# Optimization experiments

Measured on AMD Instinct MI355X. Metric: run time of the kernel, lower is better.

Reference implementation:

```python
import jax, jax.numpy as jnp
import numpy as np

B, C_IN, C_OUT, H, W = 8, 4, 64, 8, 2048


def setup_inputs() -> dict:
    key = jax.random.key(0)
    ks = jax.random.split(key, 7)
    # torch Conv2d default init: U(-s, s) with s = 1/sqrt(fan_in), fan_in = C_in*1*1
    s = 1.0 / np.sqrt(C_IN)
    u = lambda k, shape: jax.random.uniform(k, shape, jnp.float32, -s, s)
    return {
        "x": jax.random.normal(ks[0], (B, C_IN, H, W), jnp.float32),
        "Wq": u(ks[1], (C_OUT, C_IN)), "bq": u(ks[2], (C_OUT,)),
        "Wk": u(ks[3], (C_OUT, C_IN)), "bk": u(ks[4], (C_OUT,)),
        "Wv": u(ks[5], (C_OUT, C_IN)), "bv": u(ks[6], (C_OUT,)),
        "causal": 1,
    }


def reference(x, Wq, bq, Wk, bk, Wv, bv, causal):
    b, c_in, h, w = x.shape
    # 1x1 conv == per-pixel linear over channel axis
    def proj(Wm, bm):
        y = jnp.einsum('bchw,oc->bohw', x, Wm) + bm[None, :, None, None]
        return y.reshape(b, -1, w)              # [B, C_out*H, W]
    Q = proj(Wq, bq)
    K = proj(Wk, bk)
    V = proj(Wv, bv)
    d = Q.shape[1]
    # scores[b,k,l] = sum_d Q[b,d,k] * K[b,d,l] / sqrt(d)   -> [B, W, W]
    scores = jnp.einsum('bdk,bdl->bkl', Q, K) / (float(d) ** 0.5)
    if causal:
        # faithful to torch: triu zeros lower triangle, then any zero -> -inf
        scores = jnp.triu(scores)
        scores = jnp.where(scores != 0, scores, -jnp.inf)
    attn = jax.nn.softmax(scores, axis=-1)
    # x_out[b,d,k] = sum_l V[b,d,l] * attn[b,k,l]
    x_out = jnp.einsum('bdl,bkl->bdk', V, attn).reshape(b, -1, h, w)
    return x_out, scores  # plot_weight is the pre-softmax (masked) scores
```

## Files before the change

### kernel.cpp

```cpp
#include <hip/hip_runtime.h>
#include <math.h>


#define B_ 8
#define W_ 2048
#define D_ 512
#define SCALE_ 0.04419417382415922f
#define NEG_BIG_ (-3.0e38f)

typedef __attribute__((ext_vector_type(8))) short bf16x8;
typedef __attribute__((ext_vector_type(4))) float f32x4;

__device__ __forceinline__ unsigned short f2bf(float x) {
  unsigned int u = __float_as_uint(x);
  u += 0x7fffu + ((u >> 16) & 1u);
  return (unsigned short)(u >> 16);
}
__device__ __forceinline__ float bf2f(unsigned short h) {
  return __uint_as_float(((unsigned int)h) << 16);
}
__device__ __forceinline__ void split2(float x, unsigned short& hi, unsigned short& lo) {
  hi = f2bf(x);
  lo = f2bf(x - bf2f(hi));
}

__device__ __forceinline__ void gl16(const unsigned short* g, unsigned short* l) {
  __builtin_amdgcn_global_load_lds(
      (__attribute__((address_space(1))) void*)const_cast<unsigned short*>(g),
      (__attribute__((address_space(3))) void*)l, 16, 0, 0);
}

__device__ __forceinline__ int swz(int row, int lq) {
  return row * 32 + ((lq ^ ((row >> 1) & 3)) << 3);
}

__global__ __launch_bounds__(256) void proj_qk(
    const float* __restrict__ x,
    const float* __restrict__ Wq, const float* __restrict__ bq,
    const float* __restrict__ Wk, const float* __restrict__ bk,
    unsigned short* __restrict__ Qhi, unsigned short* __restrict__ Qlo,
    unsigned short* __restrict__ Khi, unsigned short* __restrict__ Klo) {
  int idx = blockIdx.x * 256 + threadIdx.x;
  int d = idx & (D_ - 1);
  int w = (idx >> 9) & (W_ - 1);
  int b = idx >> 20;
  int o = d >> 3, h = d & 7;
  const float* xp = x + (((size_t)b * 4) * 8 + h) * W_ + w;
  float x0 = xp[0], x1 = xp[8 * W_], x2 = xp[16 * W_], x3 = xp[24 * W_];
  const float* wq = Wq + o * 4;
  const float* wk = Wk + o * 4;
  float q = bq[o] + wq[0] * x0 + wq[1] * x1 + wq[2] * x2 + wq[3] * x3;
  float k = bk[o] + wk[0] * x0 + wk[1] * x1 + wk[2] * x2 + wk[3] * x3;
  unsigned short h16, l16;
  split2(q, h16, l16); Qhi[idx] = h16; Qlo[idx] = l16;
  split2(k, h16, l16); Khi[idx] = h16; Klo[idx] = l16;
}

__global__ __launch_bounds__(256) void proj_v(
    const float* __restrict__ x,
    const float* __restrict__ Wv, const float* __restrict__ bv,
    unsigned short* __restrict__ Vhi, unsigned short* __restrict__ Vlo) {
  int idx = blockIdx.x * 256 + threadIdx.x;
  int w = idx & (W_ - 1);
  int rest = idx >> 11;
  int d = rest & (D_ - 1);
  int b = rest >> 9;
  int o = d >> 3, h = d & 7;
  const float* xp = x + (((size_t)b * 4) * 8 + h) * W_ + w;
  float x0 = xp[0], x1 = xp[8 * W_], x2 = xp[16 * W_], x3 = xp[24 * W_];
  const float* wv = Wv + o * 4;
  float v = bv[o] + wv[0] * x0 + wv[1] * x1 + wv[2] * x2 + wv[3] * x3;
  unsigned short h16, l16;
  split2(v, h16, l16); Vhi[idx] = h16; Vlo[idx] = l16;
}

__global__ __launch_bounds__(256) void scores_mfma(
    const unsigned short* __restrict__ Qhi, const unsigned short* __restrict__ Qlo,
    const unsigned short* __restrict__ Khi, const unsigned short* __restrict__ Klo,
    float* __restrict__ S, const int* __restrict__ causal_p) {
  int f = (blockIdx.z * 16 + blockIdx.y) * 16 + blockIdx.x;
  int lf = (f & 7) * 256 + (f >> 3);
  int b = lf >> 8;
  int k0 = ((lf >> 4) & 15) * 128;
  int l0 = (lf & 15) * 128;
  int causal = *causal_p;
  int t = threadIdx.x;
  float* Sb = S + (size_t)b * W_ * W_;

  if (causal && (l0 + 127 < k0)) {
    float4 nb = make_float4(NEG_BIG_, NEG_BIG_, NEG_BIG_, NEG_BIG_);
    int row = t >> 1, c0 = (t & 1) * 64;
#pragma unroll
    for (int j = 0; j < 16; j++)
      *(float4*)&Sb[(size_t)(k0 + row) * W_ + l0 + c0 + j * 4] = nb;
    return;
  }

  __shared__ __align__(16) unsigned short qh_s[128 * 32], ql_s[128 * 32];
  __shared__ __align__(16) unsigned short kh_s[128 * 32], kl_s[128 * 32];

  int wave = t >> 6, lane = t & 63;
  int wk0 = (wave >> 1) * 64, wl0 = (wave & 1) * 64;
  int lr = lane & 15, lq = lane >> 4;

  const unsigned short* Qhb = Qhi + ((size_t)b * W_ + k0) * D_;
  const unsigned short* Qlb = Qlo + ((size_t)b * W_ + k0) * D_;
  const unsigned short* Khb = Khi + ((size_t)b * W_ + l0) * D_;
  const unsigned short* Klb = Klo + ((size_t)b * W_ + l0) * D_;

  int srow0 = t >> 2, sq = t & 3;
  int srow1 = srow0 + 64;
  size_t g0 = (size_t)srow0 * D_ + ((sq ^ ((srow0 >> 1) & 3)) << 3);
  size_t g1 = (size_t)srow1 * D_ + ((sq ^ ((srow1 >> 1) & 3)) << 3);
  int a0 = t * 8, a1 = t * 8 + 2048;

  f32x4 acc[4][4];
#pragma unroll
  for (int i = 0; i < 4; i++)
#pragma unroll
    for (int j = 0; j < 4; j++) acc[i][j] = (f32x4){0.f, 0.f, 0.f, 0.f};

  for (int d0 = 0; d0 < D_; d0 += 32) {
    gl16(Qhb + g0 + d0, &qh_s[a0]);
    gl16(Qhb + g1 + d0, &qh_s[a1]);
    gl16(Qlb + g0 + d0, &ql_s[a0]);
    gl16(Qlb + g1 + d0, &ql_s[a1]);
    gl16(Khb + g0 + d0, &kh_s[a0]);
    gl16(Khb + g1 + d0, &kh_s[a1]);
    gl16(Klb + g0 + d0, &kl_s[a0]);
    gl16(Klb + g1 + d0, &kl_s[a1]);
    __syncthreads();

    bf16x8 ah[4], al[4], bh[4], bl[4];
#pragma unroll
    for (int mt = 0; mt < 4; mt++) {
      int a = swz(wk0 + mt * 16 + lr, lq);
      ah[mt] = *(const bf16x8*)&qh_s[a];
      al[mt] = *(const bf16x8*)&ql_s[a];
    }
#pragma unroll
    for (int nt = 0; nt < 4; nt++) {
      int a = swz(wl0 + nt * 16 + lr, lq);
      bh[nt] = *(const bf16x8*)&kh_s[a];
      bl[nt] = *(const bf16x8*)&kl_s[a];
    }
    __builtin_amdgcn_s_setprio(1);
#pragma unroll
    for (int mt = 0; mt < 4; mt++)
#pragma unroll
      for (int nt = 0; nt < 4; nt++) {
        acc[mt][nt] = __builtin_amdgcn_mfma_f32_16x16x32_bf16(ah[mt], bh[nt], acc[mt][nt], 0, 0, 0);
        acc[mt][nt] = __builtin_amdgcn_mfma_f32_16x16x32_bf16(ah[mt], bl[nt], acc[mt][nt], 0, 0, 0);
        acc[mt][nt] = __builtin_amdgcn_mfma_f32_16x16x32_bf16(al[mt], bh[nt], acc[mt][nt], 0, 0, 0);
      }
    __builtin_amdgcn_s_setprio(0);
    __syncthreads();
  }

#pragma unroll
  for (int mt = 0; mt < 4; mt++)
#pragma unroll
    for (int nt = 0; nt < 4; nt++)
#pragma unroll
      for (int r = 0; r < 4; r++) {
        int k = k0 + wk0 + mt * 16 + lq * 4 + r;
        int l = l0 + wl0 + nt * 16 + lr;
        float s = acc[mt][nt][r] * SCALE_;
        if (causal && (l < k || s == 0.0f)) s = NEG_BIG_;
        Sb[(size_t)k * W_ + l] = s;
      }
}

__global__ __launch_bounds__(256) void softmax_stats_kernel(
    const float* __restrict__ S, float* __restrict__ mrow, float* __restrict__ invrow,
    const int* __restrict__ causal_p) {
  int row = blockIdx.x;
  int k = row & (W_ - 1);
  int causal = *causal_p;
  const float* Sr = S + (size_t)row * W_;
  int t = threadIdx.x;
  float v[8];
  if (causal && (t * 8 + 8 <= k)) {
#pragma unroll
    for (int r = 0; r < 8; r++) v[r] = NEG_BIG_;
  } else {
    *(float4*)&v[0] = *(const float4*)&Sr[t * 8];
    *(float4*)&v[4] = *(const float4*)&Sr[t * 8 + 4];
  }
  float mx = -INFINITY;
#pragma unroll
  for (int r = 0; r < 8; r++) mx = fmaxf(mx, v[r]);
#pragma unroll
  for (int off = 1; off < 64; off <<= 1) mx = fmaxf(mx, __shfl_xor(mx, off, 64));
  __shared__ float redm[4];
  __shared__ float reds[4];
  int wid = t >> 6, lane = t & 63;
  if (lane == 0) redm[wid] = mx;
  __syncthreads();
  mx = fmaxf(fmaxf(redm[0], redm[1]), fmaxf(redm[2], redm[3]));
  float sum = 0.f;
#pragma unroll
  for (int r = 0; r < 8; r++) sum += __expf(v[r] - mx);
#pragma unroll
  for (int off = 1; off < 64; off <<= 1) sum += __shfl_xor(sum, off, 64);
  if (lane == 0) reds[wid] = sum;
  __syncthreads();
  if (t == 0) {
    float s = reds[0] + reds[1] + reds[2] + reds[3];
    mrow[row] = mx;
    invrow[row] = 1.0f / s;
  }
}

__global__ __launch_bounds__(512) void out_fused(
    const unsigned short* __restrict__ Vhi, const unsigned short* __restrict__ Vlo,
    const float* __restrict__ S,
    const float* __restrict__ mrow, const float* __restrict__ invrow,
    float* __restrict__ O, const int* __restrict__ causal_p) {
  int f = blockIdx.z * 32 + blockIdx.x;
  int lf = (f & 7) * 32 + (f >> 3);
  int b = lf >> 5;
  int r5 = lf & 31;
  int k0 = (r5 >> 1) * 128;
  int dh = r5 & 1;
  int causal = *causal_p;
  int t = threadIdx.x;
  int wave = t >> 6, lane = t & 63;
  int wd0 = (wave >> 1) * 64;
  int wk0 = (wave & 1) * 64;
  int lr = lane & 15, lq = lane >> 4;

  __shared__ __align__(16) unsigned short vh_s[2][256 * 32], vl_s[2][256 * 32];
  __shared__ __align__(16) unsigned short ph_s[2][128 * 32], pl_s[2][128 * 32];

  const unsigned short* Vhb = Vhi + ((size_t)b * D_ + dh * 256) * W_;
  const unsigned short* Vlb = Vlo + ((size_t)b * D_ + dh * 256) * W_;
  const float* Sb = S + (size_t)b * W_ * W_;

  int vrow0 = t >> 2, vc = t & 3;
  int vxor = (vc ^ ((vrow0 >> 1) & 3)) << 3;
  const unsigned short* VhA = Vhb + (size_t)vrow0 * W_ + vxor;
  const unsigned short* VhB = VhA + (size_t)128 * W_;
  const unsigned short* VlA = Vlb + (size_t)vrow0 * W_ + vxor;
  const unsigned short* VlB = VlA + (size_t)128 * W_;
  int a0 = t * 8, a1 = t * 8 + 4096;

  int prow = t >> 2, pc = t & 3;
  const float* Srow = Sb + (size_t)(k0 + prow) * W_ + pc * 8;
  int paddr = prow * 32 + ((pc ^ ((prow >> 1) & 3)) << 3);
  float m = mrow[(size_t)b * W_ + k0 + prow];
  float inv = invrow[(size_t)b * W_ + k0 + prow];

  f32x4 acc[4][4];
#pragma unroll
  for (int i = 0; i < 4; i++)
#pragma unroll
    for (int j = 0; j < 4; j++) acc[i][j] = (f32x4){0.f, 0.f, 0.f, 0.f};

  int lstart = causal ? k0 : 0;
  int nch = (W_ - lstart) >> 5;

  auto stageV = [&](int buf, int l) {
    gl16(VhA + l, &vh_s[buf][a0]);
    gl16(VhB + l, &vh_s[buf][a1]);
    gl16(VlA + l, &vl_s[buf][a0]);
    gl16(VlB + l, &vl_s[buf][a1]);
  };
  auto writeP = [&](unsigned short* __restrict__ ph, unsigned short* __restrict__ pl,
                    float4 s0, float4 s1) {
    float p[8];
    p[0] = __expf(s0.x - m) * inv; p[1] = __expf(s0.y - m) * inv;
    p[2] = __expf(s0.z - m) * inv; p[3] = __expf(s0.w - m) * inv;
    p[4] = __expf(s1.x - m) * inv; p[5] = __expf(s1.y - m) * inv;
    p[6] = __expf(s1.z - m) * inv; p[7] = __expf(s1.w - m) * inv;
    unsigned short hi8[8] __attribute__((aligned(16)));
    unsigned short lo8[8] __attribute__((aligned(16)));
#pragma unroll
    for (int j = 0; j < 8; j++) split2(p[j], hi8[j], lo8[j]);
    *(uint4*)&ph[paddr] = *(uint4*)hi8;
    *(uint4*)&pl[paddr] = *(uint4*)lo8;
  };
  auto compute = [&](const unsigned short* vh, const unsigned short* vl,
                     const unsigned short* ph, const unsigned short* pl) {
    bf16x8 ah[4], al[4], bh[4], bl[4];
#pragma unroll
    for (int mt = 0; mt < 4; mt++) {
      int a = swz(wd0 + mt * 16 + lr, lq);
      ah[mt] = *(const bf16x8*)&vh[a];
      al[mt] = *(const bf16x8*)&vl[a];
    }
#pragma unroll
    for (int nt = 0; nt < 4; nt++) {
      int a = swz(wk0 + nt * 16 + lr, lq);
      bh[nt] = *(const bf16x8*)&ph[a];
      bl[nt] = *(const bf16x8*)&pl[a];
    }
    __builtin_amdgcn_s_setprio(1);
#pragma unroll
    for (int mt = 0; mt < 4; mt++)
#pragma unroll
      for (int nt = 0; nt < 4; nt++) {
        acc[mt][nt] = __builtin_amdgcn_mfma_f32_16x16x32_bf16(ah[mt], bh[nt], acc[mt][nt], 0, 0, 0);
        acc[mt][nt] = __builtin_amdgcn_mfma_f32_16x16x32_bf16(ah[mt], bl[nt], acc[mt][nt], 0, 0, 0);
        acc[mt][nt] = __builtin_amdgcn_mfma_f32_16x16x32_bf16(al[mt], bh[nt], acc[mt][nt], 0, 0, 0);
      }
    __builtin_amdgcn_s_setprio(0);
  };

  float4 sE0, sE1, sO0, sO1;

  sE0 = *(const float4*)&Srow[lstart];      sE1 = *(const float4*)&Srow[lstart + 4];
  sO0 = *(const float4*)&Srow[lstart + 32]; sO1 = *(const float4*)&Srow[lstart + 36];
  stageV(0, lstart);
  writeP(&ph_s[0][0], &pl_s[0][0], sE0, sE1);
  __syncthreads();

  for (int ci = 0; ci < nch; ci += 2) {
    int base = lstart + ci * 32;
    if (ci + 2 < nch) {
      sE0 = *(const float4*)&Srow[base + 64];
      sE1 = *(const float4*)&Srow[base + 68];
    }
    stageV(1, base + 32);
    writeP(&ph_s[1][0], &pl_s[1][0], sO0, sO1);
    compute(&vh_s[0][0], &vl_s[0][0], &ph_s[0][0], &pl_s[0][0]);
    __syncthreads();
    bool more = (ci + 2 < nch);
    if (ci + 3 < nch) {
      sO0 = *(const float4*)&Srow[base + 96];
      sO1 = *(const float4*)&Srow[base + 100];
    }
    if (more) {
      stageV(0, base + 64);
      writeP(&ph_s[0][0], &pl_s[0][0], sE0, sE1);
    }
    compute(&vh_s[1][0], &vl_s[1][0], &ph_s[1][0], &pl_s[1][0]);
    __syncthreads();
  }

#pragma unroll
  for (int mt = 0; mt < 4; mt++)
#pragma unroll
    for (int nt = 0; nt < 4; nt++)
#pragma unroll
      for (int r = 0; r < 4; r++) {
        int d = dh * 256 + wd0 + mt * 16 + lq * 4 + r;
        int k = k0 + wk0 + nt * 16 + lr;
        O[((size_t)b * D_ + d) * W_ + k] = acc[mt][nt][r];
      }
}

extern "C" void kernel_launch(void* const* d_in, const int* in_sizes, int n_in,
                              void* d_out, int out_size, void* d_ws, size_t ws_size,
                              hipStream_t stream) {
  const float* x  = (const float*)d_in[0];
  const float* Wq = (const float*)d_in[1];
  const float* bq = (const float*)d_in[2];
  const float* Wk = (const float*)d_in[3];
  const float* bk = (const float*)d_in[4];
  const float* Wv = (const float*)d_in[5];
  const float* bv = (const float*)d_in[6];
  const int* causal = (const int*)d_in[7];

  float* out = (float*)d_out;
  float* x_out = out;
  float* S = out + (size_t)B_ * D_ * W_;

  const size_t NQ = (size_t)B_ * W_ * D_;
  unsigned short* wsu = (unsigned short*)d_ws;
  unsigned short* Qhi = wsu;
  unsigned short* Qlo = wsu + NQ;
  unsigned short* Khi = wsu + 2 * NQ;
  unsigned short* Klo = wsu + 3 * NQ;
  unsigned short* Vhi = wsu + 4 * NQ;
  unsigned short* Vlo = wsu + 5 * NQ;
  float* mrow   = (float*)(wsu + 6 * NQ);
  float* invrow = mrow + (size_t)B_ * W_;

  int nproj = (int)(NQ / 256);
  proj_qk<<<nproj, 256, 0, stream>>>(x, Wq, bq, Wk, bk, Qhi, Qlo, Khi, Klo);
  proj_v<<<nproj, 256, 0, stream>>>(x, Wv, bv, Vhi, Vlo);
  scores_mfma<<<dim3(W_ / 128, W_ / 128, B_), 256, 0, stream>>>(Qhi, Qlo, Khi, Klo, S, causal);
  softmax_stats_kernel<<<B_ * W_, 256, 0, stream>>>(S, mrow, invrow, causal);
  out_fused<<<dim3(32, 1, B_), 512, 0, stream>>>(Vhi, Vlo, S, mrow, invrow, x_out, causal);
}
```

Baseline: 416.9 us.

## Fuse softmax stats into scores kernel, vectorize projections, rebalance output kernel

Per-row partial max and sum-exp are computed in the scores epilogue and written per 128-column tile. A small combine kernel merges them, which removes the separate pass that re-read the full score matrix for softmax statistics. The Q/K/V projection kernels now compute 8 outputs per thread with 16-byte vector stores instead of scalar 2-byte stores. The output kernel moves to 256-thread blocks covering 128 d-rows each, doubling the block count for better occupancy and load balance. Fully masked tiles skip the stats write, so combine_stats starts at the first valid tile to avoid reading uninitialized entries.

```diff
diff --git a/kernel.cpp b/kernel.cpp
--- a/kernel.cpp
+++ b/kernel.cpp
@@ -41,19 +41,32 @@
     unsigned short* __restrict__ Qhi, unsigned short* __restrict__ Qlo,
     unsigned short* __restrict__ Khi, unsigned short* __restrict__ Klo) {
   int idx = blockIdx.x * 256 + threadIdx.x;
-  int d = idx & (D_ - 1);
-  int w = (idx >> 9) & (W_ - 1);
-  int b = idx >> 20;
-  int o = d >> 3, h = d & 7;
-  const float* xp = x + (((size_t)b * 4) * 8 + h) * W_ + w;
-  float x0 = xp[0], x1 = xp[8 * W_], x2 = xp[16 * W_], x3 = xp[24 * W_];
-  const float* wq = Wq + o * 4;
-  const float* wk = Wk + o * 4;
-  float q = bq[o] + wq[0] * x0 + wq[1] * x1 + wq[2] * x2 + wq[3] * x3;
-  float k = bk[o] + wk[0] * x0 + wk[1] * x1 + wk[2] * x2 + wk[3] * x3;
-  unsigned short h16, l16;
-  split2(q, h16, l16); Qhi[idx] = h16; Qlo[idx] = l16;
-  split2(k, h16, l16); Khi[idx] = h16; Klo[idx] = l16;
+  int o = idx & 63;
+  int w = (idx >> 6) & (W_ - 1);
+  int b = idx >> 17;
+  const float* xb = x + (size_t)b * 32 * W_ + w;
+  float xv[4][8];
+#pragma unroll
+  for (int c = 0; c < 4; c++)
+#pragma unroll
+    for (int h = 0; h < 8; h++) xv[c][h] = xb[(c * 8 + h) * W_];
+  float wq0 = Wq[o * 4], wq1 = Wq[o * 4 + 1], wq2 = Wq[o * 4 + 2], wq3 = Wq[o * 4 + 3];
+  float wk0 = Wk[o * 4], wk1 = Wk[o * 4 + 1], wk2 = Wk[o * 4 + 2], wk3 = Wk[o * 4 + 3];
+  float bqv = bq[o], bkv = bk[o];
+  unsigned short qh8[8] __attribute__((aligned(16))), ql8[8] __attribute__((aligned(16)));
+  unsigned short kh8[8] __attribute__((aligned(16))), kl8[8] __attribute__((aligned(16)));
+#pragma unroll
+  for (int h = 0; h < 8; h++) {
+    float q = bqv + wq0 * xv[0][h] + wq1 * xv[1][h] + wq2 * xv[2][h] + wq3 * xv[3][h];
+    float k = bkv + wk0 * xv[0][h] + wk1 * xv[1][h] + wk2 * xv[2][h] + wk3 * xv[3][h];
+    split2(q, qh8[h], ql8[h]);
+    split2(k, kh8[h], kl8[h]);
+  }
+  size_t base = ((size_t)b * W_ + w) * D_ + o * 8;
+  *(uint4*)&Qhi[base] = *(uint4*)qh8;
+  *(uint4*)&Qlo[base] = *(uint4*)ql8;
+  *(uint4*)&Khi[base] = *(uint4*)kh8;
+  *(uint4*)&Klo[base] = *(uint4*)kl8;
 }
 
 __global__ __launch_bounds__(256) void proj_v(
@@ -61,23 +74,38 @@
     const float* __restrict__ Wv, const float* __restrict__ bv,
     unsigned short* __restrict__ Vhi, unsigned short* __restrict__ Vlo) {
   int idx = blockIdx.x * 256 + threadIdx.x;
-  int w = idx & (W_ - 1);
-  int rest = idx >> 11;
-  int d = rest & (D_ - 1);
-  int b = rest >> 9;
+  int wc = idx & 255;
+  int d = (idx >> 8) & (D_ - 1);
+  int b = idx >> 17;
   int o = d >> 3, h = d & 7;
-  const float* xp = x + (((size_t)b * 4) * 8 + h) * W_ + w;
-  float x0 = xp[0], x1 = xp[8 * W_], x2 = xp[16 * W_], x3 = xp[24 * W_];
-  const float* wv = Wv + o * 4;
-  float v = bv[o] + wv[0] * x0 + wv[1] * x1 + wv[2] * x2 + wv[3] * x3;
-  unsigned short h16, l16;
-  split2(v, h16, l16); Vhi[idx] = h16; Vlo[idx] = l16;
+  const float* xp = x + ((size_t)(b * 4) * 8 + h) * W_ + wc * 8;
+  float4 xa[4][2];
+#pragma unroll
+  for (int c = 0; c < 4; c++) {
+    xa[c][0] = *(const float4*)&xp[(size_t)c * 8 * W_];
+    xa[c][1] = *(const float4*)&xp[(size_t)c * 8 * W_ + 4];
+  }
+  float w0 = Wv[o * 4], w1 = Wv[o * 4 + 1], w2 = Wv[o * 4 + 2], w3 = Wv[o * 4 + 3];
+  float bvv = bv[o];
+  unsigned short vh8[8] __attribute__((aligned(16))), vl8[8] __attribute__((aligned(16)));
+#pragma unroll
+  for (int j = 0; j < 8; j++) {
+    float x0 = (j < 4) ? ((const float*)&xa[0][0])[j] : ((const float*)&xa[0][1])[j - 4];
+    float x1 = (j < 4) ? ((const float*)&xa[1][0])[j] : ((const float*)&xa[1][1])[j - 4];
+    float x2 = (j < 4) ? ((const float*)&xa[2][0])[j] : ((const float*)&xa[2][1])[j - 4];
+    float x3 = (j < 4) ? ((const float*)&xa[3][0])[j] : ((const float*)&xa[3][1])[j - 4];
+    float v = bvv + w0 * x0 + w1 * x1 + w2 * x2 + w3 * x3;
+    split2(v, vh8[j], vl8[j]);
+  }
+  size_t base = ((size_t)b * D_ + d) * W_ + wc * 8;
+  *(uint4*)&Vhi[base] = *(uint4*)vh8;
+  *(uint4*)&Vlo[base] = *(uint4*)vl8;
 }
 
 __global__ __launch_bounds__(256) void scores_mfma(
     const unsigned short* __restrict__ Qhi, const unsigned short* __restrict__ Qlo,
     const unsigned short* __restrict__ Khi, const unsigned short* __restrict__ Klo,
-    float* __restrict__ S, const int* __restrict__ causal_p) {
+    float* __restrict__ S, float2* __restrict__ stats, const int* __restrict__ causal_p) {
   int f = (blockIdx.z * 16 + blockIdx.y) * 16 + blockIdx.x;
   int lf = (f & 7) * 256 + (f >> 3);
   int b = lf >> 8;
@@ -98,6 +126,7 @@
 
   __shared__ __align__(16) unsigned short qh_s[128 * 32], ql_s[128 * 32];
   __shared__ __align__(16) unsigned short kh_s[128 * 32], kl_s[128 * 32];
+  __shared__ float sm_h[2][128], ss_h[2][128];
 
   int wave = t >> 6, lane = t & 63;
   int wk0 = (wave >> 1) * 64, wl0 = (wave & 1) * 64;
@@ -157,72 +186,67 @@
     __syncthreads();
   }
 
+  int wh = wl0 >> 6;
 #pragma unroll
   for (int mt = 0; mt < 4; mt++)
 #pragma unroll
-    for (int nt = 0; nt < 4; nt++)
-#pragma unroll
-      for (int r = 0; r < 4; r++) {
-        int k = k0 + wk0 + mt * 16 + lq * 4 + r;
+    for (int r = 0; r < 4; r++) {
+      int rr = wk0 + mt * 16 + lq * 4 + r;
+      int k = k0 + rr;
+      float v4[4];
+#pragma unroll
+      for (int nt = 0; nt < 4; nt++) {
         int l = l0 + wl0 + nt * 16 + lr;
         float s = acc[mt][nt][r] * SCALE_;
         if (causal && (l < k || s == 0.0f)) s = NEG_BIG_;
         Sb[(size_t)k * W_ + l] = s;
+        v4[nt] = s;
       }
-}
-
-__global__ __launch_bounds__(256) void softmax_stats_kernel(
-    const float* __restrict__ S, float* __restrict__ mrow, float* __restrict__ invrow,
-    const int* __restrict__ causal_p) {
-  int row = blockIdx.x;
+      float mx = fmaxf(fmaxf(v4[0], v4[1]), fmaxf(v4[2], v4[3]));
+#pragma unroll
+      for (int off = 1; off < 16; off <<= 1) mx = fmaxf(mx, __shfl_xor(mx, off, 64));
+      float ss = __expf(v4[0] - mx) + __expf(v4[1] - mx) +
+                 __expf(v4[2] - mx) + __expf(v4[3] - mx);
+#pragma unroll
+      for (int off = 1; off < 16; off <<= 1) ss += __shfl_xor(ss, off, 64);
+      if (lr == 0) { sm_h[wh][rr] = mx; ss_h[wh][rr] = ss; }
+    }
+  __syncthreads();
+  if (t < 128) {
+    float m0 = sm_h[0][t], m1 = sm_h[1][t];
+    float s0 = ss_h[0][t], s1 = ss_h[1][t];
+    float m = fmaxf(m0, m1);
+    float ssum = s0 * __expf(m0 - m) + s1 * __expf(m1 - m);
+    stats[((size_t)b * W_ + k0 + t) * 16 + (l0 >> 7)] = make_float2(m, ssum);
+  }
+}
+
+__global__ __launch_bounds__(256) void combine_stats(
+    const float2* __restrict__ stats, float* __restrict__ mrow,
+    float* __restrict__ invrow, const int* __restrict__ causal_p) {
+  int row = blockIdx.x * 256 + threadIdx.x;
   int k = row & (W_ - 1);
-  int causal = *causal_p;
-  const float* Sr = S + (size_t)row * W_;
-  int t = threadIdx.x;
-  float v[8];
-  if (causal && (t * 8 + 8 <= k)) {
-#pragma unroll
-    for (int r = 0; r < 8; r++) v[r] = NEG_BIG_;
-  } else {
-    *(float4*)&v[0] = *(const float4*)&Sr[t * 8];
-    *(float4*)&v[4] = *(const float4*)&Sr[t * 8 + 4];
-  }
-  float mx = -INFINITY;
-#pragma unroll
-  for (int r = 0; r < 8; r++) mx = fmaxf(mx, v[r]);
-#pragma unroll
-  for (int off = 1; off < 64; off <<= 1) mx = fmaxf(mx, __shfl_xor(mx, off, 64));
-  __shared__ float redm[4];
-  __shared__ float reds[4];
-  int wid = t >> 6, lane = t & 63;
-  if (lane == 0) redm[wid] = mx;
-  __syncthreads();
-  mx = fmaxf(fmaxf(redm[0], redm[1]), fmaxf(redm[2], redm[3]));
-  float sum = 0.f;
-#pragma unroll
-  for (int r = 0; r < 8; r++) sum += __expf(v[r] - mx);
-#pragma unroll
-  for (int off = 1; off < 64; off <<= 1) sum += __shfl_xor(sum, off, 64);
-  if (lane == 0) reds[wid] = sum;
-  __syncthreads();
-  if (t == 0) {
-    float s = reds[0] + reds[1] + reds[2] + reds[3];
-    mrow[row] = mx;
-    invrow[row] = 1.0f / s;
-  }
-}
-
-__global__ __launch_bounds__(512) void out_fused(
+  int lt0 = (*causal_p) ? (k >> 7) : 0;
+  const float2* sp = stats + (size_t)row * 16;
+  float m = -INFINITY;
+  for (int lt = lt0; lt < 16; lt++) m = fmaxf(m, sp[lt].x);
+  float s = 0.f;
+  for (int lt = lt0; lt < 16; lt++) s += sp[lt].y * __expf(sp[lt].x - m);
+  mrow[row] = m;
+  invrow[row] = 1.0f / s;
+}
+
+__global__ __launch_bounds__(256) void out_bal(
     const unsigned short* __restrict__ Vhi, const unsigned short* __restrict__ Vlo,
     const float* __restrict__ S,
     const float* __restrict__ mrow, const float* __restrict__ invrow,
     float* __restrict__ O, const int* __restrict__ causal_p) {
-  int f = blockIdx.z * 32 + blockIdx.x;
-  int lf = (f & 7) * 32 + (f >> 3);
-  int b = lf >> 5;
-  int r5 = lf & 31;
-  int k0 = (r5 >> 1) * 128;
-  int dh = r5 & 1;
+  int f = blockIdx.z * 64 + blockIdx.x;
+  int lf = (f & 7) * 64 + (f >> 3);
+  int b = lf >> 6;
+  int j2 = lf & 63;
+  int k0 = (j2 >> 2) * 128;
+  int dq = j2 & 3;
   int causal = *causal_p;
   int t = threadIdx.x;
   int wave = t >> 6, lane = t & 63;
@@ -230,26 +254,27 @@
   int wk0 = (wave & 1) * 64;
   int lr = lane & 15, lq = lane >> 4;
 
-  __shared__ __align__(16) unsigned short vh_s[2][256 * 32], vl_s[2][256 * 32];
+  __shared__ __align__(16) unsigned short vh_s[2][128 * 32], vl_s[2][128 * 32];
   __shared__ __align__(16) unsigned short ph_s[2][128 * 32], pl_s[2][128 * 32];
 
-  const unsigned short* Vhb = Vhi + ((size_t)b * D_ + dh * 256) * W_;
-  const unsigned short* Vlb = Vlo + ((size_t)b * D_ + dh * 256) * W_;
+  const unsigned short* Vhb = Vhi + ((size_t)b * D_ + dq * 128) * W_;
+  const unsigned short* Vlb = Vlo + ((size_t)b * D_ + dq * 128) * W_;
   const float* Sb = S + (size_t)b * W_ * W_;
 
-  int vrow0 = t >> 2, vc = t & 3;
-  int vxor = (vc ^ ((vrow0 >> 1) & 3)) << 3;
-  const unsigned short* VhA = Vhb + (size_t)vrow0 * W_ + vxor;
-  const unsigned short* VhB = VhA + (size_t)128 * W_;
-  const unsigned short* VlA = Vlb + (size_t)vrow0 * W_ + vxor;
-  const unsigned short* VlB = VlA + (size_t)128 * W_;
-  int a0 = t * 8, a1 = t * 8 + 4096;
-
-  int prow = t >> 2, pc = t & 3;
-  const float* Srow = Sb + (size_t)(k0 + prow) * W_ + pc * 8;
-  int paddr = prow * 32 + ((pc ^ ((prow >> 1) & 3)) << 3);
-  float m = mrow[(size_t)b * W_ + k0 + prow];
-  float inv = invrow[(size_t)b * W_ + k0 + prow];
+  int rA = t >> 2, qc = t & 3;
+  int vx = (qc ^ ((rA >> 1) & 3)) << 3;
+  const unsigned short* VhA = Vhb + (size_t)rA * W_ + vx;
+  const unsigned short* VhB = VhA + (size_t)64 * W_;
+  const unsigned short* VlA = Vlb + (size_t)rA * W_ + vx;
+  const unsigned short* VlB = VlA + (size_t)64 * W_;
+  int a0 = t * 8, a1 = t * 8 + 2048;
+
+  const float* SrowA = Sb + (size_t)(k0 + rA) * W_ + qc * 8;
+  const float* SrowB = SrowA + (size_t)64 * W_;
+  int pA = rA * 32 + vx;
+  int pB = pA + 64 * 32;
+  float mA = mrow[(size_t)b * W_ + k0 + rA], iA = invrow[(size_t)b * W_ + k0 + rA];
+  float mB = mrow[(size_t)b * W_ + k0 + rA + 64], iB = invrow[(size_t)b * W_ + k0 + rA + 64];
 
   f32x4 acc[4][4];
 #pragma unroll
@@ -267,18 +292,26 @@
     gl16(VlB + l, &vl_s[buf][a1]);
   };
   auto writeP = [&](unsigned short* __restrict__ ph, unsigned short* __restrict__ pl,
-                    float4 s0, float4 s1) {
+                    float4 sa0, float4 sa1, float4 sb0, float4 sb1) {
     float p[8];
-    p[0] = __expf(s0.x - m) * inv; p[1] = __expf(s0.y - m) * inv;
-    p[2] = __expf(s0.z - m) * inv; p[3] = __expf(s0.w - m) * inv;
-    p[4] = __expf(s1.x - m) * inv; p[5] = __expf(s1.y - m) * inv;
-    p[6] = __expf(s1.z - m) * inv; p[7] = __expf(s1.w - m) * inv;
     unsigned short hi8[8] __attribute__((aligned(16)));
     unsigned short lo8[8] __attribute__((aligned(16)));
+    p[0] = __expf(sa0.x - mA) * iA; p[1] = __expf(sa0.y - mA) * iA;
+    p[2] = __expf(sa0.z - mA) * iA; p[3] = __expf(sa0.w - mA) * iA;
+    p[4] = __expf(sa1.x - mA) * iA; p[5] = __expf(sa1.y - mA) * iA;
+    p[6] = __expf(sa1.z - mA) * iA; p[7] = __expf(sa1.w - mA) * iA;
 #pragma unroll
     for (int j = 0; j < 8; j++) split2(p[j], hi8[j], lo8[j]);
-    *(uint4*)&ph[paddr] = *(uint4*)hi8;
-    *(uint4*)&pl[paddr] = *(uint4*)lo8;
+    *(uint4*)&ph[pA] = *(uint4*)hi8;
+    *(uint4*)&pl[pA] = *(uint4*)lo8;
+    p[0] = __expf(sb0.x - mB) * iB; p[1] = __expf(sb0.y - mB) * iB;
+    p[2] = __expf(sb0.z - mB) * iB; p[3] = __expf(sb0.w - mB) * iB;
+    p[4] = __expf(sb1.x - mB) * iB; p[5] = __expf(sb1.y - mB) * iB;
+    p[6] = __expf(sb1.z - mB) * iB; p[7] = __expf(sb1.w - mB) * iB;
+#pragma unroll
+    for (int j = 0; j < 8; j++) split2(p[j], hi8[j], lo8[j]);
+    *(uint4*)&ph[pB] = *(uint4*)hi8;
+    *(uint4*)&pl[pB] = *(uint4*)lo8;
   };
   auto compute = [&](const unsigned short* vh, const unsigned short* vl,
                      const unsigned short* ph, const unsigned short* pl) {
@@ -307,32 +340,34 @@
     __builtin_amdgcn_s_setprio(0);
   };
 
-  float4 sE0, sE1, sO0, sO1;
-
-  sE0 = *(const float4*)&Srow[lstart];      sE1 = *(const float4*)&Srow[lstart + 4];
-  sO0 = *(const float4*)&Srow[lstart + 32]; sO1 = *(const float4*)&Srow[lstart + 36];
+  float4 sAE0, sAE1, sBE0, sBE1, sAO0, sAO1, sBO0, sBO1;
+
+  sAE0 = *(const float4*)&SrowA[lstart];      sAE1 = *(const float4*)&SrowA[lstart + 4];
+  sBE0 = *(const float4*)&SrowB[lstart];      sBE1 = *(const float4*)&SrowB[lstart + 4];
+  sAO0 = *(const float4*)&SrowA[lstart + 32]; sAO1 = *(const float4*)&SrowA[lstart + 36];
+  sBO0 = *(const float4*)&SrowB[lstart + 32]; sBO1 = *(const float4*)&SrowB[lstart + 36];
   stageV(0, lstart);
-  writeP(&ph_s[0][0], &pl_s[0][0], sE0, sE1);
+  writeP(&ph_s[0][0], &pl_s[0][0], sAE0, sAE1, sBE0, sBE1);
   __syncthreads();
 
   for (int ci = 0; ci < nch; ci += 2) {
     int base = lstart + ci * 32;
     if (ci + 2 < nch) {
-      sE0 = *(const float4*)&Srow[base + 64];
-      sE1 = *(const float4*)&Srow[base + 68];
+      sAE0 = *(const float4*)&SrowA[base + 64]; sAE1 = *(const float4*)&SrowA[base + 68];
+      sBE0 = *(const float4*)&SrowB[base + 64]; sBE1 = *(const float4*)&SrowB[base + 68];
     }
     stageV(1, base + 32);
-    writeP(&ph_s[1][0], &pl_s[1][0], sO0, sO1);
+    writeP(&ph_s[1][0], &pl_s[1][0], sAO0, sAO1, sBO0, sBO1);
     compute(&vh_s[0][0], &vl_s[0][0], &ph_s[0][0], &pl_s[0][0]);
     __syncthreads();
     bool more = (ci + 2 < nch);
     if (ci + 3 < nch) {
-      sO0 = *(const float4*)&Srow[base + 96];
-      sO1 = *(const float4*)&Srow[base + 100];
+      sAO0 = *(const float4*)&SrowA[base + 96]; sAO1 = *(const float4*)&SrowA[base + 100];
+      sBO0 = *(const float4*)&SrowB[base + 96]; sBO1 = *(const float4*)&SrowB[base + 100];
     }
     if (more) {
       stageV(0, base + 64);
-      writeP(&ph_s[0][0], &pl_s[0][0], sE0, sE1);
+      writeP(&ph_s[0][0], &pl_s[0][0], sAE0, sAE1, sBE0, sBE1);
     }
     compute(&vh_s[1][0], &vl_s[1][0], &ph_s[1][0], &pl_s[1][0]);
     __syncthreads();
@@ -344,7 +379,7 @@
     for (int nt = 0; nt < 4; nt++)
 #pragma unroll
       for (int r = 0; r < 4; r++) {
-        int d = dh * 256 + wd0 + mt * 16 + lq * 4 + r;
+        int d = dq * 128 + wd0 + mt * 16 + lq * 4 + r;
         int k = k0 + wk0 + nt * 16 + lr;
         O[((size_t)b * D_ + d) * W_ + k] = acc[mt][nt][r];
       }
@@ -376,11 +411,11 @@
   unsigned short* Vlo = wsu + 5 * NQ;
   float* mrow   = (float*)(wsu + 6 * NQ);
   float* invrow = mrow + (size_t)B_ * W_;
-
-  int nproj = (int)(NQ / 256);
-  proj_qk<<<nproj, 256, 0, stream>>>(x, Wq, bq, Wk, bk, Qhi, Qlo, Khi, Klo);
-  proj_v<<<nproj, 256, 0, stream>>>(x, Wv, bv, Vhi, Vlo);
-  scores_mfma<<<dim3(W_ / 128, W_ / 128, B_), 256, 0, stream>>>(Qhi, Qlo, Khi, Klo, S, causal);
-  softmax_stats_kernel<<<B_ * W_, 256, 0, stream>>>(S, mrow, invrow, causal);
-  out_fused<<<dim3(32, 1, B_), 512, 0, stream>>>(Vhi, Vlo, S, mrow, invrow, x_out, causal);
-}
+  float2* stats = (float2*)(invrow + (size_t)B_ * W_);
+
+  proj_qk<<<4096, 256, 0, stream>>>(x, Wq, bq, Wk, bk, Qhi, Qlo, Khi, Klo);
+  proj_v<<<4096, 256, 0, stream>>>(x, Wv, bv, Vhi, Vlo);
+  scores_mfma<<<dim3(16, 16, B_), 256, 0, stream>>>(Qhi, Qlo, Khi, Klo, S, stats, causal);
+  combine_stats<<<64, 256, 0, stream>>>(stats, mrow, invrow, causal);
+  out_bal<<<dim3(64, 1, B_), 256, 0, stream>>>(Vhi, Vlo, S, mrow, invrow, x_out, causal);
+}
```

After: 370.1 us. 11.2% less time.
